# Kernel tuning notes

Hardware: AMD Instinct MI355X
Metric: run time of the kernel (lower is better)

Reference implementation:

```python
import jax, jax.numpy as jnp
import numpy as np

N_NODES = 100000
N_EDGES = 1600000
D_IN = 64
D_OUT = 64


def setup_inputs() -> dict:
    key = jax.random.key(0)
    k1, k2, k3, k4, k5, k6 = jax.random.split(key, 6)
    feat = jax.random.normal(k1, (N_NODES, D_IN), dtype=jnp.float32)
    src = jax.random.randint(k2, (N_EDGES,), 0, N_NODES, dtype=jnp.int64)
    dst = jax.random.randint(k3, (N_EDGES,), 0, N_NODES, dtype=jnp.int64)
    edge_weight = jax.random.uniform(k4, (N_EDGES,), dtype=jnp.float32)
    # Xavier-uniform with relu gain, as in reset_parameters
    gain = float(np.sqrt(2.0))
    bound = gain * float(np.sqrt(6.0 / (D_IN + D_OUT)))
    W_neigh = jax.random.uniform(k5, (D_OUT, D_IN), dtype=jnp.float32, minval=-bound, maxval=bound)
    W_self = jax.random.uniform(k6, (D_OUT, D_IN), dtype=jnp.float32, minval=-bound, maxval=bound)
    bias = jnp.zeros((D_OUT,), dtype=jnp.float32)
    return {"feat": feat, "src": src, "dst": dst, "edge_weight": edge_weight,
            "W_neigh": W_neigh, "W_self": W_self, "bias": bias}


def reference(feat, src, dst, edge_weight, W_neigh, W_self, bias):
    n = feat.shape[0]
    # feat_drop with p=0.0 is identity; in_feats == out_feats so lin_before_mp is False
    # message: u_mul_e -> gather src features, scale by edge weight  [E, D_IN]
    m = feat[src] * edge_weight[:, None]
    # mean reduce over incoming edges (zero for isolated dst nodes, matching DGL)
    s = jax.ops.segment_sum(m, dst, num_segments=n)
    deg = jax.ops.segment_sum(jnp.ones_like(edge_weight), dst, num_segments=n)
    neigh = s / jnp.maximum(deg, 1.0)[:, None]
    h_neigh = neigh @ W_neigh.T
    h_self = feat @ W_self.T
    return h_self + h_neigh + bias
```

## Files before the change

kernel.cpp:

```cpp
#include <hip/hip_runtime.h>

constexpr int N_NODES = 100000;
constexpr int N_EDGES = 1600000;
constexpr int D = 64;

constexpr int BSH    = 6;
constexpr int BN     = 1 << BSH;
constexpr int NBUCK  = (N_NODES + BN - 1) / BN;
constexpr int NPART  = 200;
constexpr int EPB    = N_EDGES / NPART;
constexpr int CAP    = 2048;
constexpr int NCVT   = (N_NODES * D / 4) / 256;

constexpr size_t OFF_BCNT    = 0;
constexpr size_t OFF_CURSOR  = 8192;
constexpr size_t OFF_BSTART  = 16384;
constexpr size_t OFF_ENTRIES = 24576;
constexpr size_t OFF_W16     = 24576 + (size_t)N_EDGES * 8;
constexpr size_t OFF_FEAT16  = OFF_W16 + 32768;
constexpr size_t WS_NEEDED   = OFF_FEAT16 + (size_t)N_NODES * D * 2;

typedef short  bf16x8 __attribute__((ext_vector_type(8)));
typedef float  f32x4  __attribute__((ext_vector_type(4)));

__device__ __forceinline__ unsigned short f2bf(float f) {
    unsigned u = __float_as_uint(f);
    u += 0x7fffu + ((u >> 16) & 1u);
    return (unsigned short)(u >> 16);
}

__device__ __forceinline__ void split8(float4 p0, float4 p1, bf16x8& hi, bf16x8& lo) {
    float f[8] = {p0.x, p0.y, p0.z, p0.w, p1.x, p1.y, p1.z, p1.w};
#pragma unroll
    for (int i = 0; i < 8; ++i) {
        const unsigned short h = f2bf(f[i]);
        const float hf = __uint_as_float((unsigned)h << 16);
        hi[i] = (short)h;
        lo[i] = (short)f2bf(f[i] - hf);
    }
}

__global__ __launch_bounds__(256) void k_zero(int* __restrict__ bcnt) {
    int i = blockIdx.x * 256 + threadIdx.x;
    if (i < NBUCK) bcnt[i] = 0;
}

__global__ __launch_bounds__(256) void k_pre(const float4* __restrict__ feat4,
                                             unsigned short* __restrict__ feat16,
                                             const float* __restrict__ Wn,
                                             const float* __restrict__ Ws,
                                             unsigned short* __restrict__ W16,
                                             const int* __restrict__ dst,
                                             int* __restrict__ bcnt) {
    __shared__ int l[NBUCK];
    const int b   = blockIdx.x;
    const int tid = threadIdx.x;
    if (b < NCVT) {
        const int i = b * 256 + tid;
        float4 v = feat4[i];
        ushort4 o;
        o.x = f2bf(v.x); o.y = f2bf(v.y); o.z = f2bf(v.z); o.w = f2bf(v.w);
        *(ushort4*)&feat16[(size_t)i * 4] = o;
    } else if (b < NCVT + NPART) {
        const int base = (b - NCVT) * EPB;
        for (int i = tid; i < NBUCK; i += 256) l[i] = 0;
        __syncthreads();
        for (int k = tid; k < EPB; k += 256)
            atomicAdd(&l[dst[base + k] >> BSH], 1);
        __syncthreads();
        for (int i = tid; i < NBUCK; i += 256)
            if (l[i]) atomicAdd(&bcnt[i], l[i]);
    } else {
        for (int e = tid; e < D * 128; e += 256) {
            const int j = e >> 7, k = e & 127;
            const float w = (k < D) ? Ws[j * D + k] : Wn[j * D + (k - D)];
            const unsigned short h = f2bf(w);
            const float hf = __uint_as_float((unsigned)h << 16);
            W16[e] = h;
            W16[D * 128 + e] = f2bf(w - hf);
        }
    }
}

__global__ __launch_bounds__(1024) void k_scan(const int* __restrict__ bcnt,
                                               int* __restrict__ bstart,
                                               int* __restrict__ cursor) {
    __shared__ int s[1024];
    const int t  = threadIdx.x;
    const int i0 = 2 * t, i1 = 2 * t + 1;
    const int c0 = (i0 < NBUCK) ? bcnt[i0] : 0;
    const int c1 = (i1 < NBUCK) ? bcnt[i1] : 0;
    const int v  = c0 + c1;
    s[t] = v;
    __syncthreads();
    for (int off = 1; off < 1024; off <<= 1) {
        int u = (t >= off) ? s[t - off] : 0;
        __syncthreads();
        s[t] += u;
        __syncthreads();
    }
    const int excl = s[t] - v;
    if (i0 < NBUCK) { bstart[i0] = excl;      cursor[i0] = excl; }
    if (i1 < NBUCK) { bstart[i1] = excl + c0; cursor[i1] = excl + c0; }
    if (t == 0) bstart[NBUCK] = N_EDGES;
}

__global__ __launch_bounds__(256) void k_part(const int* __restrict__ src,
                                              const int* __restrict__ dst,
                                              const float* __restrict__ ew,
                                              int* __restrict__ cursor,
                                              uint2* __restrict__ entries) {
    __shared__ int l[NBUCK];
    const int tid  = threadIdx.x;
    const int base = blockIdx.x * EPB;
    for (int i = tid; i < NBUCK; i += 256) l[i] = 0;
    __syncthreads();
    for (int k = tid; k < EPB; k += 256)
        atomicAdd(&l[dst[base + k] >> BSH], 1);
    __syncthreads();
    for (int b = tid; b < NBUCK; b += 256) {
        const int c = l[b];
        l[b] = c ? atomicAdd(&cursor[b], c) : 0;
    }
    __syncthreads();
    for (int k = tid; k < EPB; k += 256) {
        const int e = base + k;
        const int d = dst[e];
        const int pos = atomicAdd(&l[d >> BSH], 1);
        entries[pos] = make_uint2((unsigned)src[e] | ((unsigned)(d & (BN - 1)) << 17),
                                  __float_as_uint(ew[e]));
    }
}

__global__ __launch_bounds__(256) void k_bucket(const uint2* __restrict__ feat16u2,
                                                const float* __restrict__ feat32,
                                                const int* __restrict__ bstart,
                                                const uint2* __restrict__ entries,
                                                const unsigned short* __restrict__ W16,
                                                const float* __restrict__ bias,
                                                float* __restrict__ out) {
    __shared__ uint2 ent[CAP];
    __shared__ __align__(16) float aggrow[BN * 68];
    __shared__ int hh[BN], st[BN], cur[BN];
    const int tid = threadIdx.x;
    const int b   = blockIdx.x;
    const int s0  = bstart[b];
    int cnt = bstart[b + 1] - s0;
    if (cnt > CAP) cnt = CAP;

    if (tid < BN) hh[tid] = 0;
    __syncthreads();
    for (int i = tid; i < cnt; i += 256)
        atomicAdd(&hh[(entries[s0 + i].x >> 17) & (BN - 1)], 1);
    __syncthreads();
    if (tid < BN) st[tid] = hh[tid];
    __syncthreads();
    for (int off = 1; off < BN; off <<= 1) {
        int u = 0;
        if (tid < BN && tid >= off) u = st[tid - off];
        __syncthreads();
        if (tid < BN) st[tid] += u;
        __syncthreads();
    }
    if (tid < BN) { const int e0 = st[tid] - hh[tid]; st[tid] = e0; cur[tid] = e0; }
    __syncthreads();
    for (int i = tid; i < cnt; i += 256) {
        uint2 e = entries[s0 + i];
        const int pos = atomicAdd(&cur[(e.x >> 17) & (BN - 1)], 1);
        ent[pos] = e;
    }
    __syncthreads();

    const int wave = tid >> 6, lane = tid & 63;
    const int group = lane >> 4, gl = lane & 15;
    for (int t = 0; t < 16; ++t) {
        const int dl  = wave * 16 + t;
        const int ss  = st[dl];
        const int deg = hh[dl];
        const int se  = ss + deg;
        float4 acc = make_float4(0.f, 0.f, 0.f, 0.f);
        for (int e = ss + group; e < se; e += 4) {
            const uint2 en = ent[e];
            const float w  = __uint_as_float(en.y);
            const uint2 p  = feat16u2[(size_t)(en.x & 0x1FFFF) * 16 + gl];
            acc.x = fmaf(__uint_as_float(p.x << 16),         w, acc.x);
            acc.y = fmaf(__uint_as_float(p.x & 0xFFFF0000u), w, acc.y);
            acc.z = fmaf(__uint_as_float(p.y << 16),         w, acc.z);
            acc.w = fmaf(__uint_as_float(p.y & 0xFFFF0000u), w, acc.w);
        }
#pragma unroll
        for (int m = 16; m <= 32; m <<= 1) {
            acc.x += __shfl_xor(acc.x, m);
            acc.y += __shfl_xor(acc.y, m);
            acc.z += __shfl_xor(acc.z, m);
            acc.w += __shfl_xor(acc.w, m);
        }
        if (group == 0) {
            const float inv = 1.0f / fmaxf((float)deg, 1.0f);
            float4 o = make_float4(acc.x * inv, acc.y * inv, acc.z * inv, acc.w * inv);
            *(float4*)&aggrow[dl * 68 + gl * 4] = o;
        }
    }
    __syncthreads();

    const int quad = lane >> 4, r = lane & 15;
    const int node0 = b * BN + wave * 16;
    int arow = node0 + r;
    if (arow > N_NODES - 1) arow = N_NODES - 1;

    bf16x8 ahi[4], alo[4];
    {
        const float* fp = &feat32[(size_t)arow * 64 + quad * 8];
        split8(*(const float4*)fp,        *(const float4*)(fp + 4),  ahi[0], alo[0]);
        split8(*(const float4*)(fp + 32), *(const float4*)(fp + 36), ahi[1], alo[1]);
        const float* ap = &aggrow[(wave * 16 + r) * 68 + quad * 8];
        split8(*(const float4*)ap,        *(const float4*)(ap + 4),  ahi[2], alo[2]);
        split8(*(const float4*)(ap + 32), *(const float4*)(ap + 36), ahi[3], alo[3]);
    }

    const unsigned short* W16lo = W16 + D * 128;
    f32x4 acc4[4] = {};
#pragma unroll
    for (int nt = 0; nt < 4; ++nt) {
#pragma unroll
        for (int kc = 0; kc < 4; ++kc) {
            const size_t wo = (size_t)(nt * 16 + r) * 128 + kc * 32 + quad * 8;
            const bf16x8 bhi = *(const bf16x8*)&W16[wo];
            const bf16x8 blo = *(const bf16x8*)&W16lo[wo];
            acc4[nt] = __builtin_amdgcn_mfma_f32_16x16x32_bf16(ahi[kc], bhi, acc4[nt], 0, 0, 0);
            acc4[nt] = __builtin_amdgcn_mfma_f32_16x16x32_bf16(alo[kc], bhi, acc4[nt], 0, 0, 0);
            acc4[nt] = __builtin_amdgcn_mfma_f32_16x16x32_bf16(ahi[kc], blo, acc4[nt], 0, 0, 0);
        }
    }

#pragma unroll
    for (int nt = 0; nt < 4; ++nt) {
        const float bv = bias[nt * 16 + r];
#pragma unroll
        for (int reg = 0; reg < 4; ++reg) {
            const int m = node0 + quad * 4 + reg;
            if (m < N_NODES) out[(size_t)m * 64 + nt * 16 + r] = acc4[nt][reg] + bv;
        }
    }
}

__global__ __launch_bounds__(256) void fb_zero(float4* __restrict__ out4,
                                               float* __restrict__ deg) {
    const int stride = gridDim.x * blockDim.x;
    int i = blockIdx.x * blockDim.x + threadIdx.x;
    const int total4 = (N_NODES * D) / 4;
    for (int idx = i; idx < total4; idx += stride)
        out4[idx] = make_float4(0.f, 0.f, 0.f, 0.f);
    for (int idx = i; idx < N_NODES; idx += stride)
        deg[idx] = 0.f;
}

__global__ __launch_bounds__(256) void fb_scatter(
    const float* __restrict__ feat, const int* __restrict__ src,
    const int* __restrict__ dst, const float* __restrict__ ew,
    float* __restrict__ out, float* __restrict__ deg) {
    const int gid  = blockIdx.x * blockDim.x + threadIdx.x;
    const int e    = gid >> 6;
    const int lane = gid & 63;
    if (e >= N_EDGES) return;
    atomicAdd(&out[(size_t)dst[e] * D + lane], feat[(size_t)src[e] * D + lane] * ew[e]);
    if (lane == 0) atomicAdd(&deg[dst[e]], 1.0f);
}

__global__ __launch_bounds__(256) void fb_finalize(
    const float* __restrict__ feat, const float* __restrict__ Wn,
    const float* __restrict__ Ws, const float* __restrict__ bias,
    const float* __restrict__ deg, float* __restrict__ out) {
    __shared__ float lWn[D * 65];
    __shared__ float lWs[D * 65];
    for (int idx = threadIdx.x; idx < D * D; idx += 256) {
        const int r = idx >> 6, c = idx & 63;
        lWn[r * 65 + c] = Wn[idx];
        lWs[r * 65 + c] = Ws[idx];
    }
    __syncthreads();
    const int wave = threadIdx.x >> 6;
    const int lane = threadIdx.x & 63;
    const int n = blockIdx.x * 4 + wave;
    if (n >= N_NODES) return;
    const float f  = feat[(size_t)n * D + lane];
    const float sv = out[(size_t)n * D + lane];
    const float inv = 1.0f / fmaxf(deg[n], 1.0f);
    float acc_s = 0.f, acc_n = 0.f;
#pragma unroll
    for (int k = 0; k < D; ++k) {
        acc_s += __shfl(f, k)  * lWs[lane * 65 + k];
        acc_n += __shfl(sv, k) * lWn[lane * 65 + k];
    }
    out[(size_t)n * D + lane] = acc_s + acc_n * inv + bias[lane];
}

extern "C" void kernel_launch(void* const* d_in, const int* in_sizes, int n_in,
                              void* d_out, int out_size, void* d_ws, size_t ws_size,
                              hipStream_t stream) {
    const float* feat = (const float*)d_in[0];
    const int*   src  = (const int*)  d_in[1];
    const int*   dst  = (const int*)  d_in[2];
    const float* ew   = (const float*)d_in[3];
    const float* Wn   = (const float*)d_in[4];
    const float* Ws   = (const float*)d_in[5];
    const float* bias = (const float*)d_in[6];
    float* out = (float*)d_out;
    char* ws = (char*)d_ws;

    if (ws_size >= WS_NEEDED) {
        int*   bcnt    = (int*)(ws + OFF_BCNT);
        int*   cursor  = (int*)(ws + OFF_CURSOR);
        int*   bstart  = (int*)(ws + OFF_BSTART);
        uint2* entries = (uint2*)(ws + OFF_ENTRIES);
        unsigned short* W16    = (unsigned short*)(ws + OFF_W16);
        unsigned short* feat16 = (unsigned short*)(ws + OFF_FEAT16);

        k_zero  <<<(NBUCK + 255) / 256, 256, 0, stream>>>(bcnt);
        k_pre   <<<NCVT + NPART + 1, 256, 0, stream>>>((const float4*)feat, feat16,
                                                       Wn, Ws, W16, dst, bcnt);
        k_scan  <<<1, 1024, 0, stream>>>(bcnt, bstart, cursor);
        k_part  <<<NPART, 256, 0, stream>>>(src, dst, ew, cursor, entries);
        k_bucket<<<NBUCK, 256, 0, stream>>>((const uint2*)feat16, feat, bstart,
                                            entries, W16, bias, out);
    } else {
        float* deg = (float*)d_ws;
        fb_zero<<<2048, 256, 0, stream>>>((float4*)out, deg);
        fb_scatter<<<(N_EDGES * 64) / 256, 256, 0, stream>>>(feat, src, dst, ew, out, deg);
        fb_finalize<<<(N_NODES + 3) / 4, 256, 0, stream>>>(feat, Wn, Ws, bias, deg, out);
    }
}
```

Before: 254.6 us.

## Split per-bucket sort into separate kernel and double edge partition blocks

Moves the per-bucket counting sort of edges by destination out of the aggregation kernel into a new k_sort kernel. k_sort writes the sorted entries and per-node start offsets to global workspace. The aggregation kernel then reads entries straight from global memory instead of LDS, which frees LDS so it can run at higher occupancy (launch bounds 256,8). It also drops the CAP truncation and doubles NPART for the partition pass. The cost is an extra kernel launch plus a round trip of all edges through global memory.

```diff
diff --git a/kernel.cpp b/kernel.cpp
--- a/kernel.cpp
+++ b/kernel.cpp
@@ -7,9 +7,8 @@
 constexpr int BSH    = 6;
 constexpr int BN     = 1 << BSH;
 constexpr int NBUCK  = (N_NODES + BN - 1) / BN;
-constexpr int NPART  = 200;
+constexpr int NPART  = 400;
 constexpr int EPB    = N_EDGES / NPART;
-constexpr int CAP    = 2048;
 constexpr int NCVT   = (N_NODES * D / 4) / 256;
 
 constexpr size_t OFF_BCNT    = 0;
@@ -18,7 +17,9 @@
 constexpr size_t OFF_ENTRIES = 24576;
 constexpr size_t OFF_W16     = 24576 + (size_t)N_EDGES * 8;
 constexpr size_t OFF_FEAT16  = OFF_W16 + 32768;
-constexpr size_t WS_NEEDED   = OFF_FEAT16 + (size_t)N_NODES * D * 2;
+constexpr size_t OFF_ENT2    = OFF_FEAT16 + (size_t)N_NODES * D * 2;
+constexpr size_t OFF_NSTART  = OFF_ENT2 + (size_t)N_EDGES * 8;
+constexpr size_t WS_NEEDED   = OFF_NSTART + ((size_t)NBUCK * BN + 1) * 4;
 
 typedef short  bf16x8 __attribute__((ext_vector_type(8)));
 typedef float  f32x4  __attribute__((ext_vector_type(4)));
@@ -132,21 +133,15 @@
     }
 }
 
-__global__ __launch_bounds__(256) void k_bucket(const uint2* __restrict__ feat16u2,
-                                                const float* __restrict__ feat32,
-                                                const int* __restrict__ bstart,
-                                                const uint2* __restrict__ entries,
-                                                const unsigned short* __restrict__ W16,
-                                                const float* __restrict__ bias,
-                                                float* __restrict__ out) {
-    __shared__ uint2 ent[CAP];
-    __shared__ __align__(16) float aggrow[BN * 68];
+__global__ __launch_bounds__(256) void k_sort(const int* __restrict__ bstart,
+                                              const uint2* __restrict__ entries,
+                                              uint2* __restrict__ entries2,
+                                              int* __restrict__ nstart) {
     __shared__ int hh[BN], st[BN], cur[BN];
     const int tid = threadIdx.x;
     const int b   = blockIdx.x;
     const int s0  = bstart[b];
-    int cnt = bstart[b + 1] - s0;
-    if (cnt > CAP) cnt = CAP;
+    const int cnt = bstart[b + 1] - s0;
 
     if (tid < BN) hh[tid] = 0;
     __syncthreads();
@@ -162,12 +157,38 @@
         if (tid < BN) st[tid] += u;
         __syncthreads();
     }
-    if (tid < BN) { const int e0 = st[tid] - hh[tid]; st[tid] = e0; cur[tid] = e0; }
+    if (tid < BN) {
+        const int e0 = st[tid] - hh[tid];
+        st[tid] = e0; cur[tid] = e0;
+        nstart[b * BN + tid] = s0 + e0;
+    }
+    if (b == NBUCK - 1 && tid == 0) nstart[NBUCK * BN] = N_EDGES;
     __syncthreads();
     for (int i = tid; i < cnt; i += 256) {
         uint2 e = entries[s0 + i];
         const int pos = atomicAdd(&cur[(e.x >> 17) & (BN - 1)], 1);
-        ent[pos] = e;
+        entries2[s0 + pos] = e;
+    }
+}
+
+__global__ __launch_bounds__(256, 8) void k_bucket(
+    const uint2* __restrict__ feat16u2,
+    const float* __restrict__ feat32,
+    const int* __restrict__ nstart,
+    const uint2* __restrict__ entries2,
+    const unsigned short* __restrict__ W16,
+    const float* __restrict__ bias,
+    float* __restrict__ out) {
+    __shared__ __align__(16) float aggrow[BN * 68];
+    __shared__ int hh[BN], st[BN];
+    const int tid = threadIdx.x;
+    const int b   = blockIdx.x;
+
+    if (tid < BN) {
+        const int s = nstart[b * BN + tid];
+        const int e = nstart[b * BN + tid + 1];
+        st[tid] = s;
+        hh[tid] = e - s;
     }
     __syncthreads();
 
@@ -180,7 +201,7 @@
         const int se  = ss + deg;
         float4 acc = make_float4(0.f, 0.f, 0.f, 0.f);
         for (int e = ss + group; e < se; e += 4) {
-            const uint2 en = ent[e];
+            const uint2 en = entries2[e];
             const float w  = __uint_as_float(en.y);
             const uint2 p  = feat16u2[(size_t)(en.x & 0x1FFFF) * 16 + gl];
             acc.x = fmaf(__uint_as_float(p.x << 16),         w, acc.x);
@@ -315,14 +336,17 @@
         uint2* entries = (uint2*)(ws + OFF_ENTRIES);
         unsigned short* W16    = (unsigned short*)(ws + OFF_W16);
         unsigned short* feat16 = (unsigned short*)(ws + OFF_FEAT16);
+        uint2* entries2 = (uint2*)(ws + OFF_ENT2);
+        int*   nstart   = (int*)(ws + OFF_NSTART);
 
         k_zero  <<<(NBUCK + 255) / 256, 256, 0, stream>>>(bcnt);
         k_pre   <<<NCVT + NPART + 1, 256, 0, stream>>>((const float4*)feat, feat16,
                                                        Wn, Ws, W16, dst, bcnt);
         k_scan  <<<1, 1024, 0, stream>>>(bcnt, bstart, cursor);
         k_part  <<<NPART, 256, 0, stream>>>(src, dst, ew, cursor, entries);
-        k_bucket<<<NBUCK, 256, 0, stream>>>((const uint2*)feat16, feat, bstart,
-                                            entries, W16, bias, out);
+        k_sort  <<<NBUCK, 256, 0, stream>>>(bstart, entries, entries2, nstart);
+        k_bucket<<<NBUCK, 256, 0, stream>>>((const uint2*)feat16, feat, nstart,
+                                            entries2, W16, bias, out);
     } else {
         float* deg = (float*)d_ws;
         fb_zero<<<2048, 256, 0, stream>>>((float4*)out, deg);
```

Result: no change. 257.9 us (+1.3%).
